# Kernel tuning notes

Hardware: AMD Instinct MI355X
Metric: run time of the kernel (lower is better)

Reference implementation:

```python
import jax, jax.numpy as jnp
import numpy as np

HEADS = 12

def setup_inputs() -> dict:
    key = jax.random.key(0)
    k1, k2, k3 = jax.random.split(key, 3)
    b, n, d = 8, 1024, 768
    x = jax.random.normal(k1, (b, n, d), dtype=jnp.float32)
    # xavier_uniform-like init for linear weights
    lim_qkv = float(np.sqrt(6.0 / (d + 3 * d)))
    W_qkv = jax.random.uniform(k2, (3 * d, d), dtype=jnp.float32, minval=-lim_qkv, maxval=lim_qkv)
    b_qkv = jnp.zeros((3 * d,), dtype=jnp.float32)
    lim_o = float(np.sqrt(6.0 / (d + d)))
    W_out = jax.random.uniform(k3, (d, d), dtype=jnp.float32, minval=-lim_o, maxval=lim_o)
    b_out = jnp.zeros((d,), dtype=jnp.float32)
    return {"x": x, "W_qkv": W_qkv, "b_qkv": b_qkv, "W_out": W_out, "b_out": b_out}

def reference(x, W_qkv, b_qkv, W_out, b_out):
    b, n, d = x.shape
    h = HEADS
    hd = d // h
    scale = d ** (-0.5)  # NOTE: original scales by dim**-0.5, not head_dim**-0.5
    qkv = x @ W_qkv.T + b_qkv                      # [b, n, 3d]
    q, k, v = jnp.split(qkv, 3, axis=-1)           # each [b, n, d]
    def to_heads(t):
        return t.reshape(b, n, h, hd).transpose(0, 2, 1, 3)  # [b, h, n, hd]
    q, k, v = to_heads(q), to_heads(k), to_heads(v)
    dots = jnp.einsum('bhid,bhjd->bhij', q, k) * scale       # [b, h, n, n]
    attn = jax.nn.softmax(dots, axis=-1)
    out = jnp.einsum('bhij,bhjd->bhid', attn, v)             # [b, h, n, hd]
    out = out.transpose(0, 2, 1, 3).reshape(b, n, d)
    return out @ W_out.T + b_out
```

## Files before the change

### kernel.cpp

```cpp
#include <hip/hip_runtime.h>
#include <stdint.h>

typedef __bf16 bf16x8 __attribute__((ext_vector_type(8)));
typedef float  f32x4  __attribute__((ext_vector_type(4)));
typedef unsigned short u16;

#define AS1 __attribute__((address_space(1)))
#define AS3 __attribute__((address_space(3)))
#define G2L(gp, lp) __builtin_amdgcn_global_load_lds( \
    (const AS1 unsigned int*)(uintptr_t)(gp), \
    (AS3 unsigned int*)(uintptr_t)(lp), 16, 0, 0)

static __device__ __forceinline__ u16 f32_to_bf16(float f) {
    unsigned u = __float_as_uint(f);
    u += 0x7fffu + ((u >> 16) & 1u);
    return (u16)(u >> 16);
}

static __device__ __forceinline__ unsigned pack_bf16(float lo, float hi) {
    return (unsigned)f32_to_bf16(lo) | ((unsigned)f32_to_bf16(hi) << 16);
}

static __device__ __forceinline__ float fast_exp2(float x) {
    return __builtin_amdgcn_exp2f(x);
}

static __device__ __forceinline__ f32x4 mfma16(bf16x8 a, bf16x8 b, f32x4 c) {
    return __builtin_amdgcn_mfma_f32_16x16x32_bf16(a, b, c, 0, 0, 0);
}

__global__ void cvt3_k(const float* __restrict__ a, const float* __restrict__ b,
                       const float* __restrict__ c, u16* __restrict__ out) {
    const int i = blockIdx.x * blockDim.x + threadIdx.x;
    const float* src; int off;
    if (i < 1572864)      { src = a; off = 0; }
    else if (i < 2015232) { src = b; off = 1572864; }
    else                  { src = c; off = 2015232; }
    const float4 v = reinterpret_cast<const float4*>(src)[i - off];
    reinterpret_cast<uint2*>(out)[i] = make_uint2(pack_bf16(v.x, v.y), pack_bf16(v.z, v.w));
}

template<int OUTF32>
__global__ __launch_bounds__(256, 3) void gemm_bt_k(const u16* __restrict__ A, const u16* __restrict__ B,
                                                    const float* __restrict__ bias, void* __restrict__ Cp,
                                                    int M, int N, int K) {
    __shared__ __align__(16) u16 As[128 * 64];
    __shared__ __align__(16) u16 Bs[128 * 64];
    const int t = threadIdx.x, w = t >> 6, l = t & 63, lr = l & 15, lg = l >> 4;
    const int wr = w >> 1, wc = w & 1;
    const long rowBase = (long)blockIdx.y * 128;
    const long colBase = (long)blockIdx.x * 128;

    const f32x4 z = {0.f, 0.f, 0.f, 0.f};
    f32x4 acc[4][4];
    #pragma unroll
    for (int m = 0; m < 4; ++m)
        #pragma unroll
        for (int n = 0; n < 4; ++n) acc[m][n] = z;

    const int kSteps = K >> 6;
    for (int kt = 0; kt < kSteps; ++kt) {
        const int k0 = kt << 6;
        __syncthreads();
        #pragma unroll
        for (int i = 0; i < 4; ++i) {
            const int c = i * 256 + t;
            const int row = c >> 3, ch = c & 7;
            const int sch = ch ^ (row & 7);
            G2L(A + (rowBase + row) * K + k0 + sch * 8, As + (i * 256 + w * 64) * 8);
            G2L(B + (colBase + row) * K + k0 + sch * 8, Bs + (i * 256 + w * 64) * 8);
        }
        __syncthreads();
        #pragma unroll
        for (int kk = 0; kk < 2; ++kk) {
            bf16x8 af[4], bfr[4];
            #pragma unroll
            for (int m = 0; m < 4; ++m) {
                const int row = wr * 64 + m * 16 + lr;
                af[m] = *reinterpret_cast<const bf16x8*>(&As[row * 64 + (((kk * 4 + lg) ^ (lr & 7)) << 3)]);
            }
            #pragma unroll
            for (int n = 0; n < 4; ++n) {
                const int row = wc * 64 + n * 16 + lr;
                bfr[n] = *reinterpret_cast<const bf16x8*>(&Bs[row * 64 + (((kk * 4 + lg) ^ (lr & 7)) << 3)]);
            }
            #pragma unroll
            for (int m = 0; m < 4; ++m)
                #pragma unroll
                for (int n = 0; n < 4; ++n) acc[m][n] = mfma16(af[m], bfr[n], acc[m][n]);
        }
    }
    #pragma unroll
    for (int n = 0; n < 4; ++n) {
        const long gc = colBase + wc * 64 + n * 16 + lr;
        const float bv = bias[gc];
        #pragma unroll
        for (int m = 0; m < 4; ++m) {
            const long gr = rowBase + wr * 64 + m * 16 + lg * 4;
            #pragma unroll
            for (int r = 0; r < 4; ++r) {
                const float v = acc[m][n][r] + bv;
                if (OUTF32) reinterpret_cast<float*>(Cp)[(gr + r) * N + gc] = v;
                else        reinterpret_cast<u16*>(Cp)[(gr + r) * N + gc] = f32_to_bf16(v);
            }
        }
    }
}

__global__ __launch_bounds__(256) void transpose_v_k(const u16* __restrict__ qkv, u16* __restrict__ vt) {
    const int bh = blockIdx.y, b = bh / 12, h = bh % 12;
    const int nt = blockIdx.x;
    __shared__ __align__(16) u16 Ts[64][72];
    const int t = threadIdx.x;
    const int rr = t >> 2;
    #pragma unroll
    for (int i = 0; i < 2; ++i) {
        const int ch = (t & 3) + i * 4;
        const u16* src = qkv + (long)(b * 1024 + nt * 64 + rr) * 2304 + 1536 + h * 64 + ch * 8;
        *reinterpret_cast<uint4*>(&Ts[rr][ch * 8]) = *reinterpret_cast<const uint4*>(src);
    }
    __syncthreads();
    #pragma unroll
    for (int i = 0; i < 2; ++i) {
        const int ch = (t & 3) + i * 4;
        u16 vals[8];
        #pragma unroll
        for (int j = 0; j < 8; ++j)
            vals[j] = Ts[(j & 3) * 16 + ch * 2 + (j >> 2)][rr];
        u16* dst = vt + (long)(bh * 64 + rr) * 1024 + nt * 64 + ch * 8;
        *reinterpret_cast<uint4*>(dst) = *reinterpret_cast<const uint4*>(vals);
    }
}

__global__ __launch_bounds__(256, 2) void attn_k(const u16* __restrict__ qkv, const u16* __restrict__ vt,
                                                 u16* __restrict__ outp) {
    const int id = blockIdx.x;
    const int bh = id % 96, qt = id / 96;
    const int b = bh / 12, h = bh % 12;
    const int t = threadIdx.x, w = t >> 6, l = t & 63, lr = l & 15, lg = l >> 4;
    __shared__ __align__(16) u16 Ks[2][64 * 64];
    __shared__ __align__(16) u16 Vts[2][64 * 64];
    __shared__ __align__(16) u16 Ps[4 * 16 * 64];

    const u16* kb = qkv + 768 + h * 64;
    const u16* vb = vt + (long)bh * 64 * 1024;

    #pragma unroll
    for (int i = 0; i < 2; ++i) {
        const int c = (i * 4 + w) * 64 + l;
        const int row = c >> 3, sch = (c & 7) ^ (row & 7);
        G2L(kb + (long)(b * 1024 + row) * 2304 + sch * 8, &Ks[0][(i * 4 + w) * 512]);
        G2L(vb + (long)row * 1024 + sch * 8, &Vts[0][(i * 4 + w) * 512]);
    }
    #pragma unroll
    for (int j = 0; j < 2; ++j) {
        const int c = j * 256 + t, row = c >> 3, ch = c & 7;
        const uint4 q = *reinterpret_cast<const uint4*>(
            qkv + (long)(b * 1024 + qt * 64 + row) * 2304 + h * 64 + ch * 8);
        *reinterpret_cast<uint4*>(&Ps[row * 64 + ((ch ^ (row & 7)) << 3)]) = q;
    }
    __syncthreads();
    bf16x8 aq[2];
    #pragma unroll
    for (int kk = 0; kk < 2; ++kk)
        aq[kk] = *reinterpret_cast<const bf16x8*>(&Ps[(w * 16 + lr) * 64 + (((kk * 4 + lg) ^ (lr & 7)) << 3)]);

    const f32x4 z = {0.f, 0.f, 0.f, 0.f};
    f32x4 o[4] = {z, z, z, z};
    float lacc[4] = {0.f, 0.f, 0.f, 0.f};
    const float sc2 = 0.052058773f;

    for (int kt = 0; kt < 16; ++kt) {
        const int cur = kt & 1;
        asm volatile("s_waitcnt vmcnt(0)" ::: "memory");
        __builtin_amdgcn_sched_barrier(0);
        __builtin_amdgcn_s_barrier();
        __builtin_amdgcn_sched_barrier(0);
        if (kt < 15) {
            const int ktn = kt + 1;
            #pragma unroll
            for (int i = 0; i < 2; ++i) {
                const int c = (i * 4 + w) * 64 + l;
                const int row = c >> 3, sch = (c & 7) ^ (row & 7);
                G2L(kb + (long)(b * 1024 + ktn * 64 + row) * 2304 + sch * 8, &Ks[cur ^ 1][(i * 4 + w) * 512]);
                G2L(vb + (long)row * 1024 + ktn * 64 + sch * 8, &Vts[cur ^ 1][(i * 4 + w) * 512]);
            }
        }
        __builtin_amdgcn_sched_barrier(0);
        f32x4 s[4] = {z, z, z, z};
        #pragma unroll
        for (int kk = 0; kk < 2; ++kk) {
            #pragma unroll
            for (int kc = 0; kc < 4; ++kc) {
                const int row = kc * 16 + lr;
                bf16x8 bk = *reinterpret_cast<const bf16x8*>(&Ks[cur][row * 64 + (((kk * 4 + lg) ^ (lr & 7)) << 3)]);
                s[kc] = mfma16(aq[kk], bk, s[kc]);
            }
        }
        #pragma unroll
        for (int r = 0; r < 4; ++r) {
            const float p0 = fast_exp2(s[0][r] * sc2);
            const float p1 = fast_exp2(s[1][r] * sc2);
            const float p2 = fast_exp2(s[2][r] * sc2);
            const float p3 = fast_exp2(s[3][r] * sc2);
            lacc[r] += (p0 + p1) + (p2 + p3);
            const unsigned w0 = pack_bf16(p0, p1);
            const unsigned w1 = pack_bf16(p2, p3);
            const int q = lg * 4 + r;
            const int csw = (lr >> 1) ^ (q & 7);
            *reinterpret_cast<uint2*>(&Ps[w * 1024 + q * 64 + csw * 8 + (lr & 1) * 4]) = make_uint2(w0, w1);
        }
        #pragma unroll
        for (int kk = 0; kk < 2; ++kk) {
            bf16x8 pa = *reinterpret_cast<const bf16x8*>(&Ps[w * 1024 + lr * 64 + (((kk * 4 + lg) ^ (lr & 7)) << 3)]);
            #pragma unroll
            for (int n = 0; n < 4; ++n) {
                const int row = n * 16 + lr;
                bf16x8 vbf = *reinterpret_cast<const bf16x8*>(&Vts[cur][row * 64 + (((kk * 4 + lg) ^ (lr & 7)) << 3)]);
                o[n] = mfma16(pa, vbf, o[n]);
            }
        }
    }
    #pragma unroll
    for (int r = 0; r < 4; ++r) {
        float rs = lacc[r];
        #pragma unroll
        for (int off = 1; off < 16; off <<= 1) rs += __shfl_xor(rs, off, 64);
        lacc[r] = rs;
    }
    const int qrow = qt * 64 + w * 16 + lg * 4;
    #pragma unroll
    for (int n = 0; n < 4; ++n) {
        #pragma unroll
        for (int r = 0; r < 4; ++r) {
            const float v = o[n][r] / lacc[r];
            outp[(long)(b * 1024 + qrow + r) * 768 + h * 64 + n * 16 + lr] = f32_to_bf16(v);
        }
    }
}

extern "C" void kernel_launch(void* const* d_in, const int* in_sizes, int n_in,
                              void* d_out, int out_size, void* d_ws, size_t ws_size,
                              hipStream_t stream) {
    (void)in_sizes; (void)n_in; (void)out_size; (void)ws_size;
    const float* x    = (const float*)d_in[0];
    const float* Wqkv = (const float*)d_in[1];
    const float* bqkv = (const float*)d_in[2];
    const float* Wout = (const float*)d_in[3];
    const float* bout = (const float*)d_in[4];

    u16* xb   = (u16*)d_ws;
    u16* Wqb  = xb  + 6291456;
    u16* Wob  = Wqb + 1769472;
    u16* qkv  = Wob + 589824;
    u16* vtb  = qkv + 18874368;
    u16* attn = vtb + 6291456;

    cvt3_k<<<8448, 256, 0, stream>>>(x, Wqkv, Wout, xb);

    gemm_bt_k<0><<<dim3(18, 64), 256, 0, stream>>>(xb, Wqb, bqkv, qkv, 8192, 2304, 768);
    transpose_v_k<<<dim3(16, 96), 256, 0, stream>>>(qkv, vtb);
    attn_k<<<1536, 256, 0, stream>>>(qkv, vtb, attn);
    gemm_bt_k<1><<<dim3(6, 64), 256, 0, stream>>>(attn, Wob, bout, d_out, 8192, 768, 768);
}
```

Before: 121.7 us.

## Double-buffer GEMM, swizzle block order, and split-K attention across waves

```diff
diff --git a/kernel.cpp b/kernel.cpp
--- a/kernel.cpp
+++ b/kernel.cpp
@@ -41,15 +41,19 @@
 }
 
 template<int OUTF32>
-__global__ __launch_bounds__(256, 3) void gemm_bt_k(const u16* __restrict__ A, const u16* __restrict__ B,
+__global__ __launch_bounds__(256, 2) void gemm_bt_k(const u16* __restrict__ A, const u16* __restrict__ B,
                                                     const float* __restrict__ bias, void* __restrict__ Cp,
-                                                    int M, int N, int K) {
-    __shared__ __align__(16) u16 As[128 * 64];
-    __shared__ __align__(16) u16 Bs[128 * 64];
+                                                    int M, int N, int K, int nbx) {
+    __shared__ __align__(16) u16 As[2][128 * 64];
+    __shared__ __align__(16) u16 Bs[2][128 * 64];
+    const int id = blockIdx.x;
+    const int cpx = gridDim.x >> 3;
+    const int swz = (id & 7) * cpx + (id >> 3);
+    const int bx = swz % nbx, by = swz / nbx;
     const int t = threadIdx.x, w = t >> 6, l = t & 63, lr = l & 15, lg = l >> 4;
     const int wr = w >> 1, wc = w & 1;
-    const long rowBase = (long)blockIdx.y * 128;
-    const long colBase = (long)blockIdx.x * 128;
+    const long rowBase = (long)by * 128;
+    const long colBase = (long)bx * 128;
 
     const f32x4 z = {0.f, 0.f, 0.f, 0.f};
     f32x4 acc[4][4];
@@ -59,30 +63,42 @@
         for (int n = 0; n < 4; ++n) acc[m][n] = z;
 
     const int kSteps = K >> 6;
+    #pragma unroll
+    for (int i = 0; i < 4; ++i) {
+        const int c = i * 256 + t, row = c >> 3, ch = c & 7;
+        const int sch = ch ^ (row & 7);
+        G2L(A + (rowBase + row) * K + sch * 8, &As[0][(i * 256 + w * 64) * 8]);
+        G2L(B + (colBase + row) * K + sch * 8, &Bs[0][(i * 256 + w * 64) * 8]);
+    }
     for (int kt = 0; kt < kSteps; ++kt) {
-        const int k0 = kt << 6;
-        __syncthreads();
-        #pragma unroll
-        for (int i = 0; i < 4; ++i) {
-            const int c = i * 256 + t;
-            const int row = c >> 3, ch = c & 7;
-            const int sch = ch ^ (row & 7);
-            G2L(A + (rowBase + row) * K + k0 + sch * 8, As + (i * 256 + w * 64) * 8);
-            G2L(B + (colBase + row) * K + k0 + sch * 8, Bs + (i * 256 + w * 64) * 8);
-        }
-        __syncthreads();
+        const int cur = kt & 1;
+        asm volatile("s_waitcnt vmcnt(0)" ::: "memory");
+        __builtin_amdgcn_sched_barrier(0);
+        __builtin_amdgcn_s_barrier();
+        __builtin_amdgcn_sched_barrier(0);
+        if (kt + 1 < kSteps) {
+            const int k0 = (kt + 1) << 6;
+            #pragma unroll
+            for (int i = 0; i < 4; ++i) {
+                const int c = i * 256 + t, row = c >> 3, ch = c & 7;
+                const int sch = ch ^ (row & 7);
+                G2L(A + (rowBase + row) * K + k0 + sch * 8, &As[cur ^ 1][(i * 256 + w * 64) * 8]);
+                G2L(B + (colBase + row) * K + k0 + sch * 8, &Bs[cur ^ 1][(i * 256 + w * 64) * 8]);
+            }
+        }
+        __builtin_amdgcn_sched_barrier(0);
         #pragma unroll
         for (int kk = 0; kk < 2; ++kk) {
             bf16x8 af[4], bfr[4];
             #pragma unroll
             for (int m = 0; m < 4; ++m) {
                 const int row = wr * 64 + m * 16 + lr;
-                af[m] = *reinterpret_cast<const bf16x8*>(&As[row * 64 + (((kk * 4 + lg) ^ (lr & 7)) << 3)]);
+                af[m] = *reinterpret_cast<const bf16x8*>(&As[cur][row * 64 + (((kk * 4 + lg) ^ (lr & 7)) << 3)]);
             }
             #pragma unroll
             for (int n = 0; n < 4; ++n) {
                 const int row = wc * 64 + n * 16 + lr;
-                bfr[n] = *reinterpret_cast<const bf16x8*>(&Bs[row * 64 + (((kk * 4 + lg) ^ (lr & 7)) << 3)]);
+                bfr[n] = *reinterpret_cast<const bf16x8*>(&Bs[cur][row * 64 + (((kk * 4 + lg) ^ (lr & 7)) << 3)]);
             }
             #pragma unroll
             for (int m = 0; m < 4; ++m)
@@ -126,115 +142,125 @@
         u16 vals[8];
         #pragma unroll
         for (int j = 0; j < 8; ++j)
-            vals[j] = Ts[(j & 3) * 16 + ch * 2 + (j >> 2)][rr];
+            vals[j] = Ts[(ch >> 2) * 32 + (j >> 2) * 16 + (ch & 3) * 4 + (j & 3)][rr];
         u16* dst = vt + (long)(bh * 64 + rr) * 1024 + nt * 64 + ch * 8;
         *reinterpret_cast<uint4*>(dst) = *reinterpret_cast<const uint4*>(vals);
     }
 }
 
-__global__ __launch_bounds__(256, 2) void attn_k(const u16* __restrict__ qkv, const u16* __restrict__ vt,
+__global__ __launch_bounds__(256, 1) void attn_k(const u16* __restrict__ qkv, const u16* __restrict__ vt,
                                                  u16* __restrict__ outp) {
     const int id = blockIdx.x;
     const int bh = id % 96, qt = id / 96;
     const int b = bh / 12, h = bh % 12;
     const int t = threadIdx.x, w = t >> 6, l = t & 63, lr = l & 15, lg = l >> 4;
-    __shared__ __align__(16) u16 Ks[2][64 * 64];
-    __shared__ __align__(16) u16 Vts[2][64 * 64];
-    __shared__ __align__(16) u16 Ps[4 * 16 * 64];
-
-    const u16* kb = qkv + 768 + h * 64;
+    __shared__ __align__(16) float red[4 * 64 * 68 + 4 * 64];
+
+    const u16* qb = qkv + (long)(b * 1024 + qt * 64) * 2304 + h * 64;
+    bf16x8 aq[4][2];
+    #pragma unroll
+    for (int qf = 0; qf < 4; ++qf)
+        #pragma unroll
+        for (int kk = 0; kk < 2; ++kk)
+            aq[qf][kk] = *reinterpret_cast<const bf16x8*>(qb + (long)(qf * 16 + lr) * 2304 + (kk * 4 + lg) * 8);
+
+    const u16* kb = qkv + (long)(b * 1024) * 2304 + 768 + h * 64;
     const u16* vb = vt + (long)bh * 64 * 1024;
 
-    #pragma unroll
-    for (int i = 0; i < 2; ++i) {
-        const int c = (i * 4 + w) * 64 + l;
-        const int row = c >> 3, sch = (c & 7) ^ (row & 7);
-        G2L(kb + (long)(b * 1024 + row) * 2304 + sch * 8, &Ks[0][(i * 4 + w) * 512]);
-        G2L(vb + (long)row * 1024 + sch * 8, &Vts[0][(i * 4 + w) * 512]);
-    }
-    #pragma unroll
-    for (int j = 0; j < 2; ++j) {
-        const int c = j * 256 + t, row = c >> 3, ch = c & 7;
-        const uint4 q = *reinterpret_cast<const uint4*>(
-            qkv + (long)(b * 1024 + qt * 64 + row) * 2304 + h * 64 + ch * 8);
-        *reinterpret_cast<uint4*>(&Ps[row * 64 + ((ch ^ (row & 7)) << 3)]) = q;
-    }
-    __syncthreads();
-    bf16x8 aq[2];
-    #pragma unroll
-    for (int kk = 0; kk < 2; ++kk)
-        aq[kk] = *reinterpret_cast<const bf16x8*>(&Ps[(w * 16 + lr) * 64 + (((kk * 4 + lg) ^ (lr & 7)) << 3)]);
-
     const f32x4 z = {0.f, 0.f, 0.f, 0.f};
-    f32x4 o[4] = {z, z, z, z};
+    f32x4 o[4][4];
+    #pragma unroll
+    for (int qf = 0; qf < 4; ++qf)
+        #pragma unroll
+        for (int n = 0; n < 4; ++n) o[qf][n] = z;
     float lacc[4] = {0.f, 0.f, 0.f, 0.f};
     const float sc2 = 0.052058773f;
 
-    for (int kt = 0; kt < 16; ++kt) {
-        const int cur = kt & 1;
-        asm volatile("s_waitcnt vmcnt(0)" ::: "memory");
-        __builtin_amdgcn_sched_barrier(0);
-        __builtin_amdgcn_s_barrier();
-        __builtin_amdgcn_sched_barrier(0);
-        if (kt < 15) {
-            const int ktn = kt + 1;
-            #pragma unroll
-            for (int i = 0; i < 2; ++i) {
-                const int c = (i * 4 + w) * 64 + l;
-                const int row = c >> 3, sch = (c & 7) ^ (row & 7);
-                G2L(kb + (long)(b * 1024 + ktn * 64 + row) * 2304 + sch * 8, &Ks[cur ^ 1][(i * 4 + w) * 512]);
-                G2L(vb + (long)row * 1024 + ktn * 64 + sch * 8, &Vts[cur ^ 1][(i * 4 + w) * 512]);
-            }
-        }
-        __builtin_amdgcn_sched_barrier(0);
-        f32x4 s[4] = {z, z, z, z};
-        #pragma unroll
-        for (int kk = 0; kk < 2; ++kk) {
-            #pragma unroll
-            for (int kc = 0; kc < 4; ++kc) {
-                const int row = kc * 16 + lr;
-                bf16x8 bk = *reinterpret_cast<const bf16x8*>(&Ks[cur][row * 64 + (((kk * 4 + lg) ^ (lr & 7)) << 3)]);
-                s[kc] = mfma16(aq[kk], bk, s[kc]);
-            }
-        }
-        #pragma unroll
-        for (int r = 0; r < 4; ++r) {
-            const float p0 = fast_exp2(s[0][r] * sc2);
-            const float p1 = fast_exp2(s[1][r] * sc2);
-            const float p2 = fast_exp2(s[2][r] * sc2);
-            const float p3 = fast_exp2(s[3][r] * sc2);
-            lacc[r] += (p0 + p1) + (p2 + p3);
-            const unsigned w0 = pack_bf16(p0, p1);
-            const unsigned w1 = pack_bf16(p2, p3);
-            const int q = lg * 4 + r;
-            const int csw = (lr >> 1) ^ (q & 7);
-            *reinterpret_cast<uint2*>(&Ps[w * 1024 + q * 64 + csw * 8 + (lr & 1) * 4]) = make_uint2(w0, w1);
-        }
-        #pragma unroll
-        for (int kk = 0; kk < 2; ++kk) {
-            bf16x8 pa = *reinterpret_cast<const bf16x8*>(&Ps[w * 1024 + lr * 64 + (((kk * 4 + lg) ^ (lr & 7)) << 3)]);
-            #pragma unroll
-            for (int n = 0; n < 4; ++n) {
-                const int row = n * 16 + lr;
-                bf16x8 vbf = *reinterpret_cast<const bf16x8*>(&Vts[cur][row * 64 + (((kk * 4 + lg) ^ (lr & 7)) << 3)]);
-                o[n] = mfma16(pa, vbf, o[n]);
-            }
-        }
-    }
+    #pragma unroll
+    for (int ti = 0; ti < 4; ++ti) {
+        const int kt = ti * 4 + w;
+        bf16x8 bk[4][2], vv[2][4];
+        #pragma unroll
+        for (int kc = 0; kc < 4; ++kc)
+            #pragma unroll
+            for (int kk = 0; kk < 2; ++kk)
+                bk[kc][kk] = *reinterpret_cast<const bf16x8*>(
+                    kb + (long)(kt * 64 + kc * 16 + lr) * 2304 + (kk * 4 + lg) * 8);
+        #pragma unroll
+        for (int kk = 0; kk < 2; ++kk)
+            #pragma unroll
+            for (int n = 0; n < 4; ++n)
+                vv[kk][n] = *reinterpret_cast<const bf16x8*>(
+                    vb + (long)(n * 16 + lr) * 1024 + kt * 64 + (kk * 4 + lg) * 8);
+        f32x4 s[4][4];
+        #pragma unroll
+        for (int kc = 0; kc < 4; ++kc)
+            #pragma unroll
+            for (int qf = 0; qf < 4; ++qf) s[kc][qf] = z;
+        #pragma unroll
+        for (int kk = 0; kk < 2; ++kk)
+            #pragma unroll
+            for (int kc = 0; kc < 4; ++kc)
+                #pragma unroll
+                for (int qf = 0; qf < 4; ++qf)
+                    s[kc][qf] = mfma16(bk[kc][kk], aq[qf][kk], s[kc][qf]);
+        bf16x8 pa[4][2];
+        #pragma unroll
+        for (int qf = 0; qf < 4; ++qf) {
+            float pv[4][4];
+            #pragma unroll
+            for (int kc = 0; kc < 4; ++kc)
+                #pragma unroll
+                for (int r = 0; r < 4; ++r) {
+                    pv[kc][r] = fast_exp2(s[kc][qf][r] * sc2);
+                    lacc[qf] += pv[kc][r];
+                }
+            uint4 u0, u1;
+            u0.x = pack_bf16(pv[0][0], pv[0][1]); u0.y = pack_bf16(pv[0][2], pv[0][3]);
+            u0.z = pack_bf16(pv[1][0], pv[1][1]); u0.w = pack_bf16(pv[1][2], pv[1][3]);
+            u1.x = pack_bf16(pv[2][0], pv[2][1]); u1.y = pack_bf16(pv[2][2], pv[2][3]);
+            u1.z = pack_bf16(pv[3][0], pv[3][1]); u1.w = pack_bf16(pv[3][2], pv[3][3]);
+            pa[qf][0] = *reinterpret_cast<bf16x8*>(&u0);
+            pa[qf][1] = *reinterpret_cast<bf16x8*>(&u1);
+        }
+        #pragma unroll
+        for (int kk = 0; kk < 2; ++kk)
+            #pragma unroll
+            for (int n = 0; n < 4; ++n)
+                #pragma unroll
+                for (int qf = 0; qf < 4; ++qf)
+                    o[qf][n] = mfma16(pa[qf][kk], vv[kk][n], o[qf][n]);
+    }
+    #pragma unroll
+    for (int qf = 0; qf < 4; ++qf) {
+        lacc[qf] += __shfl_xor(lacc[qf], 16, 64);
+        lacc[qf] += __shfl_xor(lacc[qf], 32, 64);
+    }
+    float* ored = red;
+    float* dnm = red + 4 * 64 * 68;
+    #pragma unroll
+    for (int qf = 0; qf < 4; ++qf)
+        #pragma unroll
+        for (int n = 0; n < 4; ++n)
+            #pragma unroll
+            for (int r = 0; r < 4; ++r)
+                ored[(w * 64 + qf * 16 + lg * 4 + r) * 68 + n * 16 + lr] = o[qf][n][r];
+    if (l < 16) {
+        #pragma unroll
+        for (int qf = 0; qf < 4; ++qf) dnm[w * 64 + qf * 16 + lr] = lacc[qf];
+    }
+    __syncthreads();
     #pragma unroll
     for (int r = 0; r < 4; ++r) {
-        float rs = lacc[r];
-        #pragma unroll
-        for (int off = 1; off < 16; off <<= 1) rs += __shfl_xor(rs, off, 64);
-        lacc[r] = rs;
-    }
-    const int qrow = qt * 64 + w * 16 + lg * 4;
-    #pragma unroll
-    for (int n = 0; n < 4; ++n) {
-        #pragma unroll
-        for (int r = 0; r < 4; ++r) {
-            const float v = o[n][r] / lacc[r];
-            outp[(long)(b * 1024 + qrow + r) * 768 + h * 64 + n * 16 + lr] = f32_to_bf16(v);
+        const int q = w * 16 + lg * 4 + r;
+        const float dq = dnm[q] + dnm[64 + q] + dnm[128 + q] + dnm[192 + q];
+        const float inv = 1.0f / dq;
+        #pragma unroll
+        for (int n = 0; n < 4; ++n) {
+            const int d = n * 16 + lr;
+            const float sum = ored[q * 68 + d] + ored[(64 + q) * 68 + d]
+                            + ored[(128 + q) * 68 + d] + ored[(192 + q) * 68 + d];
+            outp[(long)(b * 1024 + qt * 64 + q) * 768 + h * 64 + d] = f32_to_bf16(sum * inv);
         }
     }
 }
@@ -258,8 +284,8 @@
 
     cvt3_k<<<8448, 256, 0, stream>>>(x, Wqkv, Wout, xb);
 
-    gemm_bt_k<0><<<dim3(18, 64), 256, 0, stream>>>(xb, Wqb, bqkv, qkv, 8192, 2304, 768);
+    gemm_bt_k<0><<<1152, 256, 0, stream>>>(xb, Wqb, bqkv, qkv, 8192, 2304, 768, 18);
     transpose_v_k<<<dim3(16, 96), 256, 0, stream>>>(qkv, vtb);
     attn_k<<<1536, 256, 0, stream>>>(qkv, vtb, attn);
-    gemm_bt_k<1><<<dim3(6, 64), 256, 0, stream>>>(attn, Wob, bout, d_out, 8192, 768, 768);
-}
+    gemm_bt_k<1><<<384, 256, 0, stream>>>(attn, Wob, bout, d_out, 8192, 768, 768, 6);
+}
```

Measured after the change: 139.6 us. +14.7%, slower.
